# Kernel optimization log

Hardware: AMD Instinct MI355X
Metric: run time of the kernel (lower is better)

The kernel has to match this reference:

```python
import jax, jax.numpy as jnp
import numpy as np

N = 4096
D = 256
H = 8
HD = D // H
EPS = 1e-5
NEG = -1e9


def layer_norm(x, g, b):
    mu = jnp.mean(x, axis=-1, keepdims=True)
    var = jnp.mean(jnp.square(x - mu), axis=-1, keepdims=True)
    return (x - mu) * jax.lax.rsqrt(var + EPS) * g + b


def setup_inputs() -> dict:
    key = jax.random.key(0)
    ks = jax.random.split(key, 12)
    s = 1.0 / np.sqrt(D)
    inp = {
        "x": jax.random.normal(ks[0], (N, D), dtype=jnp.float32),
        "adj": jax.random.randint(ks[1], (N, N), 0, 2, dtype=jnp.int32),
        "Wq": jax.random.uniform(ks[2], (D, D), jnp.float32, -s, s),
        "Wk": jax.random.uniform(ks[3], (D, D), jnp.float32, -s, s),
        "Wv": jax.random.uniform(ks[4], (D, D), jnp.float32, -s, s),
        "bq": jnp.zeros((D,), jnp.float32),
        "bk": jnp.zeros((D,), jnp.float32),
        "bv": jnp.zeros((D,), jnp.float32),
        "Wo": jax.random.uniform(ks[5], (D, D), jnp.float32, -s, s),
        "bo": jnp.zeros((D,), jnp.float32),
        "g1": jnp.ones((D,), jnp.float32),
        "beta1": jnp.zeros((D,), jnp.float32),
        "W1": jax.random.uniform(ks[6], (2 * D, D), jnp.float32, -s, s),
        "b1": jnp.zeros((2 * D,), jnp.float32),
        "W2": jax.random.uniform(ks[7], (D, 2 * D), jnp.float32, -1.0 / np.sqrt(2 * D), 1.0 / np.sqrt(2 * D)),
        "b2": jnp.zeros((D,), jnp.float32),
        "g2": jnp.ones((D,), jnp.float32),
        "beta2": jnp.zeros((D,), jnp.float32),
    }
    return inp


def reference(x, adj, Wq, Wk, Wv, bq, bk, bv, Wo, bo, g1, beta1, W1, b1, W2, b2, g2, beta2):
    n = adj.shape[0]
    # allowed = adj + I > 0 ; attention only over neighbors + self-loop
    allowed = (adj + jnp.eye(n, dtype=adj.dtype)) > 0  # (n, n) bool

    q = (x @ Wq.T + bq).reshape(n, H, HD)
    k = (x @ Wk.T + bk).reshape(n, H, HD)
    v = (x @ Wv.T + bv).reshape(n, H, HD)

    scale = 1.0 / np.sqrt(HD)
    scores = jnp.einsum('nhd,mhd->hnm', q, k) * scale  # (H, n, n)
    scores = jnp.where(allowed[None, :, :], scores, NEG)
    attn = jax.nn.softmax(scores, axis=-1)
    o = jnp.einsum('hnm,mhd->nhd', attn, v).reshape(n, D)
    h = o @ Wo.T + bo

    x = layer_norm(x + h, g1, beta1)
    ffn = jax.nn.relu(x @ W1.T + b1) @ W2.T + b2
    x = layer_norm(x + ffn, g2, beta2)
    return x
```

## Files before the change

### kernel.cpp

```cpp
#include <hip/hip_runtime.h>
#include <hip/hip_bf16.h>

typedef __attribute__((ext_vector_type(4))) float f32x4;
typedef __attribute__((ext_vector_type(8))) short s16x8;

#define NROWS 4096
#define DMODEL 256
#define NHEAD 8
#define HDIM 32
#define PSTRIDE 72
#define OSTRIDE 33
#define M2C 24.0f
#define NM (NROWS * DMODEL)
#define SA_S 264
#define SH_S 268
#define SY_S 264
#define SR_S 520

__device__ __forceinline__ short bf16r(float f) {
    union { float f; unsigned u; } v; v.f = f;
    unsigned r = v.u + 0x7fffu + ((v.u >> 16) & 1u);
    return (short)(r >> 16);
}

__device__ __forceinline__ float fexp2(float x) {
    float r;
    asm("v_exp_f32 %0, %1" : "=v"(r) : "v"(x));
    return r;
}

__device__ __forceinline__ unsigned pk_bf16(float a, float b) {
#if __has_builtin(__builtin_amdgcn_cvt_pk_bf16_f32)
    typedef __bf16 bf2 __attribute__((ext_vector_type(2)));
    union { bf2 h; unsigned u; } c;
    c.h = __builtin_amdgcn_cvt_pk_bf16_f32(a, b);
    return c.u;
#else
    return (unsigned)(unsigned short)bf16r(a) | ((unsigned)(unsigned short)bf16r(b) << 16);
#endif
}

__device__ __forceinline__ s16x8 pack8(float4 a, float4 b) {
    s16x8 r;
    r[0] = bf16r(a.x); r[1] = bf16r(a.y); r[2] = bf16r(a.z); r[3] = bf16r(a.w);
    r[4] = bf16r(b.x); r[5] = bf16r(b.y); r[6] = bf16r(b.z); r[7] = bf16r(b.w);
    return r;
}

__global__ __launch_bounds__(256) void qkvprep_kernel(
        const float* __restrict__ X,
        const float* __restrict__ Wq, const float* __restrict__ Wk,
        const float* __restrict__ Wv,
        const float* __restrict__ bq, const float* __restrict__ bk,
        const float* __restrict__ bv,
        const int* __restrict__ adj, unsigned* __restrict__ mask,
        const float* __restrict__ Wo, const float* __restrict__ W1,
        const float* __restrict__ W2, short* __restrict__ Wb,
        short* __restrict__ Qb, short* __restrict__ Kb,
        short* __restrict__ Vtb) {
    __shared__ short sT[64 * 72];
    const int b = blockIdx.x;
    const int tid = threadIdx.x;
    const int lane = tid & 63;
    if (b < 768) {
        const int wv = tid >> 6;
        const int quad = lane >> 4, col = lane & 15;
        const int bx = b & 63, by = b >> 6;
        const int o0 = by * 64;
        const int z = o0 >> 8;
        const float* Wsrc = (z == 0) ? Wq : (z == 1 ? Wk : Wv);
        const float* bias = (z == 0) ? bq : (z == 1 ? bk : bv);
        const int ow0 = o0 & 255;
        const int n0 = bx * 64 + wv * 16;
        const float QSC = 0.25505653437397888f;

        f32x4 zero = {0.f, 0.f, 0.f, 0.f};
        f32x4 acc[4] = {zero, zero, zero, zero};
        const float* ap = X + (size_t)(n0 + col) * DMODEL + quad * 8;
#pragma unroll
        for (int k0 = 0; k0 < DMODEL; k0 += 32) {
            float4 a0 = *(const float4*)(ap + k0);
            float4 a1 = *(const float4*)(ap + k0 + 4);
            s16x8 af = pack8(a0, a1);
#pragma unroll
            for (int t = 0; t < 4; ++t) {
                const float* wp = Wsrc + (size_t)(ow0 + t * 16 + col) * DMODEL + quad * 8 + k0;
                s16x8 bf = pack8(*(const float4*)wp, *(const float4*)(wp + 4));
                acc[t] = __builtin_amdgcn_mfma_f32_16x16x32_bf16(af, bf, acc[t], 0, 0, 0);
            }
        }
        if (z != 2) {
#pragma unroll
            for (int t = 0; t < 4; ++t) {
                const int oo = ow0 + t * 16 + col;
                float bvv = bias[oo];
#pragma unroll
                for (int r = 0; r < 4; ++r) {
                    int n = n0 + quad * 4 + r;
                    float v = acc[t][r] + bvv;
                    if (z == 0) Qb[(size_t)n * DMODEL + oo] = bf16r(v * QSC);
                    else        Kb[(size_t)(oo >> 5) * NROWS * HDIM + (size_t)n * HDIM + (oo & 31)] = bf16r(v);
                }
            }
        } else {
#pragma unroll
            for (int t = 0; t < 4; ++t) {
                const int oot = t * 16 + col;
                float bvv = bias[ow0 + oot];
#pragma unroll
                for (int r = 0; r < 4; ++r) {
                    int nn = wv * 16 + quad * 4 + r;
                    sT[oot * 72 + nn] = bf16r(acc[t][r] + bvv);
                }
            }
            __syncthreads();
            const int oor = tid >> 2, nseg = (tid & 3) * 16;
            s16x8 v0 = *(const s16x8*)&sT[oor * 72 + nseg];
            s16x8 v1 = *(const s16x8*)&sT[oor * 72 + nseg + 8];
            short* dst = Vtb + (size_t)(ow0 + oor) * NROWS + bx * 64 + nseg;
            *(s16x8*)dst = v0;
            *(s16x8*)(dst + 8) = v1;
        }
    } else if (b < 2816) {
        const int waveid = (b - 768) * 4 + (tid >> 6);
        int4 av[8];
        int rows[8], segs[8];
#pragma unroll
        for (int i = 0; i < 8; ++i) {
            const int task = waveid + i * 8192;
            rows[i] = task >> 4; segs[i] = task & 15;
            av[i] = *(const int4*)(adj + (size_t)rows[i] * NROWS + segs[i] * 256 + lane * 4);
        }
#pragma unroll
        for (int i = 0; i < 8; ++i) {
            const int row = rows[i];
            const int c0 = segs[i] * 256 + lane * 4;
            unsigned nib = (unsigned)(av[i].x > 0 || c0 == row)
                         | ((unsigned)(av[i].y > 0 || c0 + 1 == row) << 1)
                         | ((unsigned)(av[i].z > 0 || c0 + 2 == row) << 2)
                         | ((unsigned)(av[i].w > 0 || c0 + 3 == row) << 3);
            unsigned v = nib << ((lane & 7) * 4);
            v |= __shfl_xor((int)v, 1, 64);
            v |= __shfl_xor((int)v, 2, 64);
            v |= __shfl_xor((int)v, 4, 64);
            if ((lane & 7) == 0)
                mask[row * 128 + segs[i] * 8 + (lane >> 3)] = v;
        }
    } else {
        int i = (b - 2816) * 2048 + tid * 8;
        const float* src; int off;
        if (i < 65536)       { src = Wo; off = i; }
        else if (i < 196608) { src = W1; off = i - 65536; }
        else                 { src = W2; off = i - 196608; }
        float4 a = *(const float4*)(src + off);
        float4 c = *(const float4*)(src + off + 4);
        *(s16x8*)(Wb + i) = pack8(a, c);
    }
}

__global__ __launch_bounds__(256) void attn_kernel(const short* __restrict__ Qb,
                                                   const short* __restrict__ Kb,
                                                   const short* __restrict__ Vtb,
                                                   const unsigned* __restrict__ mask,
                                                   float* __restrict__ Opart,
                                                   float* __restrict__ lpart) {
    __shared__ union {
        short sP[2][16 * PSTRIDE];
        float sO[HDIM][OSTRIDE];
    } u[4];
    __shared__ float sl[4][32];

    const int tid = threadIdx.x;
    const int wv = tid >> 6, lane = tid & 63;
    const int quad = lane >> 4, col = lane & 15;
    const int khalf = blockIdx.x & 1;
    const int h = (blockIdx.x >> 1) & 7;
    const int q0 = (blockIdx.x >> 4) * 32;
    const int kw = khalf * 2048 + wv * 512;

    s16x8 qf[2];
    qf[0] = *(const s16x8*)(Qb + (size_t)(q0 + col) * DMODEL + h * HDIM + quad * 8);
    qf[1] = *(const s16x8*)(Qb + (size_t)(q0 + 16 + col) * DMODEL + h * HDIM + quad * 8);

    const short* kp  = Kb + (size_t)h * NROWS * HDIM + (size_t)(kw + col) * HDIM + quad * 8;
    const short* vp0 = Vtb + (size_t)(h * HDIM + col) * NROWS + kw + quad * 8;
    const short* vp1 = vp0 + (size_t)16 * NROWS;
    const unsigned* mp0 = mask + (size_t)(q0 + col) * 128 + (kw >> 5);
    const unsigned* mp1 = mp0 + 16 * 128;

    f32x4 zero = {0.f, 0.f, 0.f, 0.f};
    f32x4 acc[2][2] = {{zero, zero}, {zero, zero}};
    float rs[2] = {0.f, 0.f};

#pragma unroll 2
    for (int it = 0; it < 8; ++it) {
        const short* k = kp + it * 64 * HDIM;
        s16x8 kf0 = *(const s16x8*)(k);
        s16x8 kf1 = *(const s16x8*)(k + 16 * HDIM);
        s16x8 kf2 = *(const s16x8*)(k + 32 * HDIM);
        s16x8 kf3 = *(const s16x8*)(k + 48 * HDIM);
        uint2 w0 = *(const uint2*)(mp0 + it * 2);
        uint2 w1 = *(const uint2*)(mp1 + it * 2);
        const short* v0 = vp0 + it * 64;
        const short* v1 = vp1 + it * 64;
        s16x8 vf00 = *(const s16x8*)(v0);
        s16x8 vf01 = *(const s16x8*)(v0 + 32);
        s16x8 vf10 = *(const s16x8*)(v1);
        s16x8 vf11 = *(const s16x8*)(v1 + 32);

#pragma unroll
        for (int qs = 0; qs < 2; ++qs) {
            unsigned wlo = (qs ? w1.x : w0.x) >> (quad * 4);
            unsigned whi = (qs ? w1.y : w0.y) >> (quad * 4);
            f32x4 st[4];
            st[0] = __builtin_amdgcn_mfma_f32_16x16x32_bf16(kf0, qf[qs], zero, 0, 0, 0);
            st[1] = __builtin_amdgcn_mfma_f32_16x16x32_bf16(kf1, qf[qs], zero, 0, 0, 0);
            st[2] = __builtin_amdgcn_mfma_f32_16x16x32_bf16(kf2, qf[qs], zero, 0, 0, 0);
            st[3] = __builtin_amdgcn_mfma_f32_16x16x32_bf16(kf3, qf[qs], zero, 0, 0, 0);

            float p[4][4];
            float r0 = 0.f;
#pragma unroll
            for (int t = 0; t < 4; ++t) {
                unsigned wm = (t < 2) ? wlo : whi;
#pragma unroll
                for (int r = 0; r < 4; ++r) {
                    float e = fexp2(st[t][r] - M2C);
                    bool ok = (wm & (1u << ((t & 1) * 16 + r))) != 0u;
                    p[t][r] = ok ? e : 0.f;
                    r0 += p[t][r];
                }
            }
            rs[qs] += r0;

            short* pb = &u[wv].sP[qs][0];
#pragma unroll
            for (int t = 0; t < 4; ++t) {
                uint2 pr;
                pr.x = pk_bf16(p[t][0], p[t][1]);
                pr.y = pk_bf16(p[t][2], p[t][3]);
                *(uint2*)(pb + col * PSTRIDE + t * 16 + quad * 4) = pr;
            }
            s16x8 pb0 = *(const s16x8*)(pb + col * PSTRIDE + quad * 8);
            s16x8 pb1 = *(const s16x8*)(pb + col * PSTRIDE + 32 + quad * 8);

            acc[qs][0] = __builtin_amdgcn_mfma_f32_16x16x32_bf16(vf00, pb0, acc[qs][0], 0, 0, 0);
            acc[qs][0] = __builtin_amdgcn_mfma_f32_16x16x32_bf16(vf01, pb1, acc[qs][0], 0, 0, 0);
            acc[qs][1] = __builtin_amdgcn_mfma_f32_16x16x32_bf16(vf10, pb0, acc[qs][1], 0, 0, 0);
            acc[qs][1] = __builtin_amdgcn_mfma_f32_16x16x32_bf16(vf11, pb1, acc[qs][1], 0, 0, 0);
        }
    }

#pragma unroll
    for (int qs = 0; qs < 2; ++qs) {
        float r = rs[qs];
        r += __shfl_xor(r, 16, 64);
        r += __shfl_xor(r, 32, 64);
        if (lane < 16) sl[wv][qs * 16 + col] = r;
#pragma unroll
        for (int rr = 0; rr < 4; ++rr) {
            u[wv].sO[quad * 4 + rr][qs * 16 + col]      = acc[qs][0][rr];
            u[wv].sO[16 + quad * 4 + rr][qs * 16 + col] = acc[qs][1][rr];
        }
    }
    __syncthreads();

    const int q = tid >> 3, hd0 = (tid & 7) * 4;
    float l = sl[0][q] + sl[1][q] + sl[2][q] + sl[3][q];
    float4 ov;
    ov.x = u[0].sO[hd0][q]     + u[1].sO[hd0][q]     + u[2].sO[hd0][q]     + u[3].sO[hd0][q];
    ov.y = u[0].sO[hd0 + 1][q] + u[1].sO[hd0 + 1][q] + u[2].sO[hd0 + 1][q] + u[3].sO[hd0 + 1][q];
    ov.z = u[0].sO[hd0 + 2][q] + u[1].sO[hd0 + 2][q] + u[2].sO[hd0 + 2][q] + u[3].sO[hd0 + 2][q];
    ov.w = u[0].sO[hd0 + 3][q] + u[1].sO[hd0 + 3][q] + u[2].sO[hd0 + 3][q] + u[3].sO[hd0 + 3][q];
    *(float4*)(Opart + (size_t)khalf * NM + (size_t)(q0 + q) * DMODEL + h * HDIM + hd0) = ov;
    if ((tid & 7) == 0) lpart[khalf * NROWS * NHEAD + (q0 + q) * NHEAD + h] = l;
}

__global__ __launch_bounds__(512) void mega_kernel(
        const float* __restrict__ Opart, const float* __restrict__ lpart,
        const float* __restrict__ X,
        const short* __restrict__ Wob, const short* __restrict__ W1b,
        const short* __restrict__ W2b,
        const float* __restrict__ bo,
        const float* __restrict__ g1, const float* __restrict__ be1,
        const float* __restrict__ b1, const float* __restrict__ b2,
        const float* __restrict__ g2, const float* __restrict__ be2,
        float* __restrict__ out) {
    __shared__ union { short sA[16 * SA_S]; short sR[16 * SR_S]; } uu;
    __shared__ float sH[16 * SH_S];
    __shared__ short sY[16 * SY_S];

    const int tid = threadIdx.x;
    const int wv = tid >> 6, lane = tid & 63;
    const int quad = lane >> 4, col = lane & 15;
    const int n0 = blockIdx.x * 16;
    const int rr_ = tid >> 5, c8 = (tid & 31) * 8;
    const int n_ln = n0 + rr_;
    f32x4 zero = {0.f, 0.f, 0.f, 0.f};

    {
        const int head = c8 >> 5;
        float li = 1.f / (lpart[(size_t)n_ln * NHEAD + head] +
                          lpart[(size_t)NROWS * NHEAD + (size_t)n_ln * NHEAD + head]);
        const float* p0 = Opart + (size_t)n_ln * DMODEL + c8;
        const float* p1 = p0 + NM;
        float4 a0 = ((const float4*)p0)[0], a1 = ((const float4*)p0)[1];
        float4 b0 = ((const float4*)p1)[0], b1v = ((const float4*)p1)[1];
        s16x8 w;
        *((unsigned*)&w + 0) = pk_bf16((a0.x + b0.x) * li, (a0.y + b0.y) * li);
        *((unsigned*)&w + 1) = pk_bf16((a0.z + b0.z) * li, (a0.w + b0.w) * li);
        *((unsigned*)&w + 2) = pk_bf16((a1.x + b1v.x) * li, (a1.y + b1v.y) * li);
        *((unsigned*)&w + 3) = pk_bf16((a1.z + b1v.z) * li, (a1.w + b1v.w) * li);
        *(s16x8*)&uu.sA[rr_ * SA_S + c8] = w;
    }
    __syncthreads();

    {
        const int o0 = wv * 32;
        f32x4 acc[2] = {zero, zero};
#pragma unroll
        for (int k0 = 0; k0 < DMODEL; k0 += 32) {
            s16x8 af = *(const s16x8*)&uu.sA[col * SA_S + k0 + quad * 8];
#pragma unroll
            for (int t = 0; t < 2; ++t) {
                s16x8 bf = *(const s16x8*)(Wob + (size_t)(o0 + t * 16 + col) * DMODEL + k0 + quad * 8);
                acc[t] = __builtin_amdgcn_mfma_f32_16x16x32_bf16(af, bf, acc[t], 0, 0, 0);
            }
        }
#pragma unroll
        for (int t = 0; t < 2; ++t) {
            int o = o0 + t * 16 + col;
            float bv = bo[o];
#pragma unroll
            for (int r = 0; r < 4; ++r)
                sH[(quad * 4 + r) * SH_S + o] = acc[t][r] + bv;
        }
    }
    __syncthreads();

    float y1v[8];
    {
        const float* xp = X + (size_t)n_ln * DMODEL + c8;
        float v[8];
        float s = 0.f;
#pragma unroll
        for (int j = 0; j < 2; ++j) {
            float4 xv = ((const float4*)xp)[j];
            float4 hv = *(const float4*)&sH[rr_ * SH_S + c8 + j * 4];
            v[j * 4 + 0] = xv.x + hv.x; v[j * 4 + 1] = xv.y + hv.y;
            v[j * 4 + 2] = xv.z + hv.z; v[j * 4 + 3] = xv.w + hv.w;
            s += v[j * 4] + v[j * 4 + 1] + v[j * 4 + 2] + v[j * 4 + 3];
        }
#pragma unroll
        for (int m = 1; m < 32; m <<= 1) s += __shfl_xor(s, m, 64);
        float mean = s * (1.f / 256.f);
        float q = 0.f;
#pragma unroll
        for (int i = 0; i < 8; ++i) { v[i] -= mean; q += v[i] * v[i]; }
#pragma unroll
        for (int m = 1; m < 32; m <<= 1) q += __shfl_xor(q, m, 64);
        float rstd = rsqrtf(q * (1.f / 256.f) + 1e-5f);
        const float* gp = g1 + c8;
        const float* bp = be1 + c8;
        s16x8 w;
#pragma unroll
        for (int j = 0; j < 2; ++j) {
            float4 gv = ((const float4*)gp)[j];
            float4 bev = ((const float4*)bp)[j];
            float a0 = v[j * 4 + 0] * rstd * gv.x + bev.x;
            float a1 = v[j * 4 + 1] * rstd * gv.y + bev.y;
            float a2 = v[j * 4 + 2] * rstd * gv.z + bev.z;
            float a3 = v[j * 4 + 3] * rstd * gv.w + bev.w;
            y1v[j * 4 + 0] = a0; y1v[j * 4 + 1] = a1;
            y1v[j * 4 + 2] = a2; y1v[j * 4 + 3] = a3;
            *((unsigned*)&w + j * 2 + 0) = pk_bf16(a0, a1);
            *((unsigned*)&w + j * 2 + 1) = pk_bf16(a2, a3);
        }
        *(s16x8*)&sY[rr_ * SY_S + c8] = w;
    }
    __syncthreads();

    {
        const int o0 = wv * 64;
        f32x4 acc[4] = {zero, zero, zero, zero};
#pragma unroll
        for (int k0 = 0; k0 < DMODEL; k0 += 32) {
            s16x8 af = *(const s16x8*)&sY[col * SY_S + k0 + quad * 8];
#pragma unroll
            for (int t = 0; t < 4; ++t) {
                s16x8 bf = *(const s16x8*)(W1b + (size_t)(o0 + t * 16 + col) * DMODEL + k0 + quad * 8);
                acc[t] = __builtin_amdgcn_mfma_f32_16x16x32_bf16(af, bf, acc[t], 0, 0, 0);
            }
        }
#pragma unroll
        for (int t = 0; t < 4; ++t) {
            int o = o0 + t * 16 + col;
            float bv = b1[o];
#pragma unroll
            for (int r = 0; r < 4; ++r)
                uu.sR[(quad * 4 + r) * SR_S + o] = bf16r(fmaxf(acc[t][r] + bv, 0.f));
        }
    }
    __syncthreads();

    {
        const int o0 = wv * 32;
        f32x4 acc[2] = {zero, zero};
#pragma unroll
        for (int k0 = 0; k0 < 512; k0 += 32) {
            s16x8 af = *(const s16x8*)&uu.sR[col * SR_S + k0 + quad * 8];
#pragma unroll
            for (int t = 0; t < 2; ++t) {
                s16x8 bf = *(const s16x8*)(W2b + (size_t)(o0 + t * 16 + col) * 512 + k0 + quad * 8);
                acc[t] = __builtin_amdgcn_mfma_f32_16x16x32_bf16(af, bf, acc[t], 0, 0, 0);
            }
        }
#pragma unroll
        for (int t = 0; t < 2; ++t) {
            int o = o0 + t * 16 + col;
            float bv = b2[o];
#pragma unroll
            for (int r = 0; r < 4; ++r)
                sH[(quad * 4 + r) * SH_S + o] = acc[t][r] + bv;
        }
    }
    __syncthreads();

    {
        float v[8];
        float s = 0.f;
#pragma unroll
        for (int j = 0; j < 2; ++j) {
            float4 hv = *(const float4*)&sH[rr_ * SH_S + c8 + j * 4];
            v[j * 4 + 0] = y1v[j * 4 + 0] + hv.x; v[j * 4 + 1] = y1v[j * 4 + 1] + hv.y;
            v[j * 4 + 2] = y1v[j * 4 + 2] + hv.z; v[j * 4 + 3] = y1v[j * 4 + 3] + hv.w;
            s += v[j * 4] + v[j * 4 + 1] + v[j * 4 + 2] + v[j * 4 + 3];
        }
#pragma unroll
        for (int m = 1; m < 32; m <<= 1) s += __shfl_xor(s, m, 64);
        float mean = s * (1.f / 256.f);
        float q = 0.f;
#pragma unroll
        for (int i = 0; i < 8; ++i) { v[i] -= mean; q += v[i] * v[i]; }
#pragma unroll
        for (int m = 1; m < 32; m <<= 1) q += __shfl_xor(q, m, 64);
        float rstd = rsqrtf(q * (1.f / 256.f) + 1e-5f);
        const float* gp = g2 + c8;
        const float* bp = be2 + c8;
        float* op = out + (size_t)n_ln * DMODEL + c8;
#pragma unroll
        for (int j = 0; j < 2; ++j) {
            float4 gv = ((const float4*)gp)[j];
            float4 bev = ((const float4*)bp)[j];
            float4 y;
            y.x = v[j * 4 + 0] * rstd * gv.x + bev.x;
            y.y = v[j * 4 + 1] * rstd * gv.y + bev.y;
            y.z = v[j * 4 + 2] * rstd * gv.z + bev.z;
            y.w = v[j * 4 + 3] * rstd * gv.w + bev.w;
            ((float4*)op)[j] = y;
        }
    }
}

extern "C" void kernel_launch(void* const* d_in, const int* in_sizes, int n_in,
                              void* d_out, int out_size, void* d_ws, size_t ws_size,
                              hipStream_t stream) {
    const float* x   = (const float*)d_in[0];
    const int*   adj = (const int*)d_in[1];
    const float* Wq  = (const float*)d_in[2];
    const float* Wk  = (const float*)d_in[3];
    const float* Wv  = (const float*)d_in[4];
    const float* bq  = (const float*)d_in[5];
    const float* bk  = (const float*)d_in[6];
    const float* bv  = (const float*)d_in[7];
    const float* Wo  = (const float*)d_in[8];
    const float* bo  = (const float*)d_in[9];
    const float* g1  = (const float*)d_in[10];
    const float* be1 = (const float*)d_in[11];
    const float* W1  = (const float*)d_in[12];
    const float* b1  = (const float*)d_in[13];
    const float* W2  = (const float*)d_in[14];
    const float* b2  = (const float*)d_in[15];
    const float* g2  = (const float*)d_in[16];
    const float* be2 = (const float*)d_in[17];
    float* out = (float*)d_out;

    char* p = (char*)d_ws;
    unsigned* mask = (unsigned*)p; p += (size_t)NROWS * 128 * 4;
    short* Wb    = (short*)p;      p += (size_t)327680 * 2;
    short* Qb    = (short*)p;      p += (size_t)NM * 2;
    short* Kb    = (short*)p;      p += (size_t)NM * 2;
    short* Vtb   = (short*)p;      p += (size_t)NM * 2;
    float* Opart = (float*)p;      p += (size_t)2 * NM * 4;
    float* lpart = (float*)p;      p += (size_t)2 * NROWS * NHEAD * 4;

    qkvprep_kernel<<<dim3(2976), dim3(256), 0, stream>>>(
        x, Wq, Wk, Wv, bq, bk, bv, adj, mask, Wo, W1, W2, Wb, Qb, Kb, Vtb);
    attn_kernel<<<dim3(2048), dim3(256), 0, stream>>>(Qb, Kb, Vtb, mask, Opart, lpart);
    mega_kernel<<<dim3(256), dim3(512), 0, stream>>>(
        Opart, lpart, x, Wb, Wb + 65536, Wb + 196608,
        bo, g1, be1, b1, b2, g2, be2, out);
}
```

Baseline: 232.4 us.

## Swizzle V into MFMA fragment layout and compute row sums via MFMA

The V projection is now written in a pre-swizzled fragment order, so each lane in the attention kernel loads its V operand with one contiguous 16-byte access per fragment instead of strided transposed rows. The softmax row sum is computed with extra MFMAs against a ones vector rather than with scalar adds and cross-lane shuffles. The -M2C offset is folded into the MFMA accumulator init so it is not subtracted per element. The cost is two extra MFMAs per query slice, and the sum now uses the bf16-rounded probabilities.

```diff
diff --git a/kernel.cpp b/kernel.cpp
--- a/kernel.cpp
+++ b/kernel.cpp
@@ -57,7 +57,7 @@
         const float* __restrict__ Wo, const float* __restrict__ W1,
         const float* __restrict__ W2, short* __restrict__ Wb,
         short* __restrict__ Qb, short* __restrict__ Kb,
-        short* __restrict__ Vtb) {
+        short* __restrict__ Vswz) {
     __shared__ short sT[64 * 72];
     const int b = blockIdx.x;
     const int tid = threadIdx.x;
@@ -114,12 +114,19 @@
                 }
             }
             __syncthreads();
-            const int oor = tid >> 2, nseg = (tid & 3) * 16;
-            s16x8 v0 = *(const s16x8*)&sT[oor * 72 + nseg];
-            s16x8 v1 = *(const s16x8*)&sT[oor * 72 + nseg + 8];
-            short* dst = Vtb + (size_t)(ow0 + oor) * NROWS + bx * 64 + nseg;
-            *(s16x8*)dst = v0;
-            *(s16x8*)(dst + 8) = v1;
+            const int f = tid >> 5;
+            const int lh = f >> 2, hdh = (f >> 1) & 1, kh = f & 1;
+            const int L0 = (tid & 31) * 2;
+            const int hgl = (ow0 >> 5) + lh;
+            short* dst = Vswz + (((size_t)(hgl * 64 + bx) * 4 + hdh * 2 + kh) * 512);
+#pragma unroll
+            for (int e = 0; e < 2; ++e) {
+                int L = L0 + e;
+                int hd_local = lh * 32 + hdh * 16 + (L & 15);
+                int key_local = kh * 32 + ((L >> 4) * 8);
+                s16x8 v = *(const s16x8*)&sT[hd_local * 72 + key_local];
+                *(s16x8*)(dst + L * 8) = v;
+            }
         }
     } else if (b < 2816) {
         const int waveid = (b - 768) * 4 + (tid >> 6);
@@ -160,7 +167,7 @@
 
 __global__ __launch_bounds__(256) void attn_kernel(const short* __restrict__ Qb,
                                                    const short* __restrict__ Kb,
-                                                   const short* __restrict__ Vtb,
+                                                   const short* __restrict__ Vswz,
                                                    const unsigned* __restrict__ mask,
                                                    float* __restrict__ Opart,
                                                    float* __restrict__ lpart) {
@@ -182,15 +189,18 @@
     qf[0] = *(const s16x8*)(Qb + (size_t)(q0 + col) * DMODEL + h * HDIM + quad * 8);
     qf[1] = *(const s16x8*)(Qb + (size_t)(q0 + 16 + col) * DMODEL + h * HDIM + quad * 8);
 
-    const short* kp  = Kb + (size_t)h * NROWS * HDIM + (size_t)(kw + col) * HDIM + quad * 8;
-    const short* vp0 = Vtb + (size_t)(h * HDIM + col) * NROWS + kw + quad * 8;
-    const short* vp1 = vp0 + (size_t)16 * NROWS;
+    const short* kp = Kb + (size_t)h * NROWS * HDIM + (size_t)(kw + col) * HDIM + quad * 8;
+    const short* vbase = Vswz + ((size_t)(h * 64 + (kw >> 6)) * 4) * 512 + lane * 8;
     const unsigned* mp0 = mask + (size_t)(q0 + col) * 128 + (kw >> 5);
     const unsigned* mp1 = mp0 + 16 * 128;
 
+    const short onev = (col == 0) ? (short)0x3F80 : (short)0;
+    const s16x8 ones = {onev, onev, onev, onev, onev, onev, onev, onev};
+
     f32x4 zero = {0.f, 0.f, 0.f, 0.f};
     f32x4 acc[2][2] = {{zero, zero}, {zero, zero}};
-    float rs[2] = {0.f, 0.f};
+    f32x4 lacc[2] = {zero, zero};
+    const f32x4 cinit = {-M2C, -M2C, -M2C, -M2C};
 
 #pragma unroll 2
     for (int it = 0; it < 8; ++it) {
@@ -201,37 +211,33 @@
         s16x8 kf3 = *(const s16x8*)(k + 48 * HDIM);
         uint2 w0 = *(const uint2*)(mp0 + it * 2);
         uint2 w1 = *(const uint2*)(mp1 + it * 2);
-        const short* v0 = vp0 + it * 64;
-        const short* v1 = vp1 + it * 64;
-        s16x8 vf00 = *(const s16x8*)(v0);
-        s16x8 vf01 = *(const s16x8*)(v0 + 32);
-        s16x8 vf10 = *(const s16x8*)(v1);
-        s16x8 vf11 = *(const s16x8*)(v1 + 32);
+        const short* vb = vbase + it * 4 * 512;
+        s16x8 vf00 = *(const s16x8*)(vb);
+        s16x8 vf01 = *(const s16x8*)(vb + 512);
+        s16x8 vf10 = *(const s16x8*)(vb + 1024);
+        s16x8 vf11 = *(const s16x8*)(vb + 1536);
 
 #pragma unroll
         for (int qs = 0; qs < 2; ++qs) {
             unsigned wlo = (qs ? w1.x : w0.x) >> (quad * 4);
             unsigned whi = (qs ? w1.y : w0.y) >> (quad * 4);
             f32x4 st[4];
-            st[0] = __builtin_amdgcn_mfma_f32_16x16x32_bf16(kf0, qf[qs], zero, 0, 0, 0);
-            st[1] = __builtin_amdgcn_mfma_f32_16x16x32_bf16(kf1, qf[qs], zero, 0, 0, 0);
-            st[2] = __builtin_amdgcn_mfma_f32_16x16x32_bf16(kf2, qf[qs], zero, 0, 0, 0);
-            st[3] = __builtin_amdgcn_mfma_f32_16x16x32_bf16(kf3, qf[qs], zero, 0, 0, 0);
+            st[0] = __builtin_amdgcn_mfma_f32_16x16x32_bf16(kf0, qf[qs], cinit, 0, 0, 0);
+            st[1] = __builtin_amdgcn_mfma_f32_16x16x32_bf16(kf1, qf[qs], cinit, 0, 0, 0);
+            st[2] = __builtin_amdgcn_mfma_f32_16x16x32_bf16(kf2, qf[qs], cinit, 0, 0, 0);
+            st[3] = __builtin_amdgcn_mfma_f32_16x16x32_bf16(kf3, qf[qs], cinit, 0, 0, 0);
 
             float p[4][4];
-            float r0 = 0.f;
 #pragma unroll
             for (int t = 0; t < 4; ++t) {
                 unsigned wm = (t < 2) ? wlo : whi;
 #pragma unroll
                 for (int r = 0; r < 4; ++r) {
-                    float e = fexp2(st[t][r] - M2C);
+                    float e = fexp2(st[t][r]);
                     bool ok = (wm & (1u << ((t & 1) * 16 + r))) != 0u;
                     p[t][r] = ok ? e : 0.f;
-                    r0 += p[t][r];
                 }
             }
-            rs[qs] += r0;
 
             short* pb = &u[wv].sP[qs][0];
 #pragma unroll
@@ -248,15 +254,14 @@
             acc[qs][0] = __builtin_amdgcn_mfma_f32_16x16x32_bf16(vf01, pb1, acc[qs][0], 0, 0, 0);
             acc[qs][1] = __builtin_amdgcn_mfma_f32_16x16x32_bf16(vf10, pb0, acc[qs][1], 0, 0, 0);
             acc[qs][1] = __builtin_amdgcn_mfma_f32_16x16x32_bf16(vf11, pb1, acc[qs][1], 0, 0, 0);
+            lacc[qs] = __builtin_amdgcn_mfma_f32_16x16x32_bf16(ones, pb0, lacc[qs], 0, 0, 0);
+            lacc[qs] = __builtin_amdgcn_mfma_f32_16x16x32_bf16(ones, pb1, lacc[qs], 0, 0, 0);
         }
     }
 
 #pragma unroll
     for (int qs = 0; qs < 2; ++qs) {
-        float r = rs[qs];
-        r += __shfl_xor(r, 16, 64);
-        r += __shfl_xor(r, 32, 64);
-        if (lane < 16) sl[wv][qs * 16 + col] = r;
+        if (lane < 16) sl[wv][qs * 16 + col] = lacc[qs][0];
 #pragma unroll
         for (int rr = 0; rr < 4; ++rr) {
             u[wv].sO[quad * 4 + rr][qs * 16 + col]      = acc[qs][0][rr];
@@ -490,13 +495,13 @@
     short* Wb    = (short*)p;      p += (size_t)327680 * 2;
     short* Qb    = (short*)p;      p += (size_t)NM * 2;
     short* Kb    = (short*)p;      p += (size_t)NM * 2;
-    short* Vtb   = (short*)p;      p += (size_t)NM * 2;
+    short* Vswz  = (short*)p;      p += (size_t)NM * 2;
     float* Opart = (float*)p;      p += (size_t)2 * NM * 4;
     float* lpart = (float*)p;      p += (size_t)2 * NROWS * NHEAD * 4;
 
     qkvprep_kernel<<<dim3(2976), dim3(256), 0, stream>>>(
-        x, Wq, Wk, Wv, bq, bk, bv, adj, mask, Wo, W1, W2, Wb, Qb, Kb, Vtb);
-    attn_kernel<<<dim3(2048), dim3(256), 0, stream>>>(Qb, Kb, Vtb, mask, Opart, lpart);
+        x, Wq, Wk, Wv, bq, bk, bv, adj, mask, Wo, W1, W2, Wb, Qb, Kb, Vswz);
+    attn_kernel<<<dim3(2048), dim3(256), 0, stream>>>(Qb, Kb, Vswz, mask, Opart, lpart);
     mega_kernel<<<dim3(256), dim3(512), 0, stream>>>(
         Opart, lpart, x, Wb, Wb + 65536, Wb + 196608,
         bo, g1, be1, b1, b2, g2, be2, out);
```

Result: no change. 227.9 us (-1.9%).
